# Kernel optimization log

Measured on AMD Instinct MI355X. Metric: run time of the kernel, lower is better.

## Reference

```python
import jax, jax.numpy as jnp
import numpy as np

NUM_HEADS = 8
HEAD_DIM = 16


def setup_inputs() -> dict:
    key = jax.random.key(0)
    ks = jax.random.split(key, 9)
    B, S, E, H = 2, 4096, 16, 128
    sc_in = 1.0 / np.sqrt(E)
    sc_h = 1.0 / np.sqrt(H)
    return {
        "x": jax.random.normal(ks[0], (B, S, E), dtype=jnp.float32),
        "wq": jax.random.normal(ks[1], (H, E), dtype=jnp.float32) * sc_in,
        "bq": jax.random.normal(ks[2], (H,), dtype=jnp.float32) * 0.02,
        "wk": jax.random.normal(ks[3], (H, E), dtype=jnp.float32) * sc_in,
        "bk": jax.random.normal(ks[4], (H,), dtype=jnp.float32) * 0.02,
        "wv": jax.random.normal(ks[5], (H, E), dtype=jnp.float32) * sc_in,
        "bv": jax.random.normal(ks[6], (H,), dtype=jnp.float32) * 0.02,
        "wo": jax.random.normal(ks[7], (E, H), dtype=jnp.float32) * sc_h,
        "bo": jax.random.normal(ks[8], (E,), dtype=jnp.float32) * 0.02,
    }


def reference(x, wq, bq, wk, bk, wv, bv, wo, bo):
    B, S, E = x.shape
    H = wq.shape[0]
    nh, hd = NUM_HEADS, HEAD_DIM
    # QKV projections (torch Linear: y = x @ W.T + b)
    q = x @ wq.T + bq  # [B,S,H]
    k = x @ wk.T + bk
    v = x @ wv.T + bv
    # split heads -> [B,nh,S,hd]
    q = q.reshape(B, S, nh, hd).transpose(0, 2, 1, 3)
    k = k.reshape(B, S, nh, hd).transpose(0, 2, 1, 3)
    v = v.reshape(B, S, nh, hd).transpose(0, 2, 1, 3)
    # flex_attention with block_mask=None == full SDPA, scale = 1/sqrt(head_dim)
    scale = 1.0 / np.sqrt(hd)
    scores = jnp.einsum("bhqd,bhkd->bhqk", q, k) * scale  # [B,nh,S,S]
    attn = jax.nn.softmax(scores, axis=-1)
    out = jnp.einsum("bhqk,bhkd->bhqd", attn, v)  # [B,nh,S,hd]
    out = out.transpose(0, 2, 1, 3).reshape(B, S, H)
    return out @ wo.T + bo
```

## Files before the change

kernel.cpp:

```cpp
#include <hip/hip_runtime.h>
#include <hip/hip_bf16.h>
#include <math.h>

#define NH 8
#define HD 16
#define EE 16
#define HH 128
#define NCH 4
#define QR 32

typedef __attribute__((ext_vector_type(8)))  short short8;
typedef __attribute__((ext_vector_type(16))) float f32x16;
typedef __attribute__((ext_vector_type(4)))  float f32x4;

#define EXP2F(x) __builtin_amdgcn_exp2f(x)

__global__ __launch_bounds__(256) void qkv_fused(
        const float* __restrict__ x,
        const float* __restrict__ wq, const float* __restrict__ bq,
        const float* __restrict__ wk, const float* __restrict__ bk,
        const float* __restrict__ wv, const float* __restrict__ bv,
        __hip_bfloat16* __restrict__ Qb, __hip_bfloat16* __restrict__ Kb,
        __hip_bfloat16* __restrict__ Vt, int S) {
    int row0 = blockIdx.x * QR;
    int b = row0 / S, s0 = row0 - b * S;
    int tid = threadIdx.x;

    __shared__ __align__(16) float xs[QR][EE];
    __shared__ short vsb[QR][130];

    ((float*)xs)[tid]       = x[(size_t)row0 * EE + tid];
    ((float*)xs)[tid + 256] = x[(size_t)row0 * EE + tid + 256];
    __syncthreads();

    int h = tid & 127, sub = tid >> 7;
    float wqr[16], wkr[16], wvr[16];
    const float4* wq4 = (const float4*)(wq + h * EE);
    const float4* wk4 = (const float4*)(wk + h * EE);
    const float4* wv4 = (const float4*)(wv + h * EE);
#pragma unroll
    for (int j = 0; j < 4; ++j) {
        float4 a = wq4[j]; wqr[4*j]=a.x; wqr[4*j+1]=a.y; wqr[4*j+2]=a.z; wqr[4*j+3]=a.w;
        float4 c = wk4[j]; wkr[4*j]=c.x; wkr[4*j+1]=c.y; wkr[4*j+2]=c.z; wkr[4*j+3]=c.w;
        float4 d = wv4[j]; wvr[4*j]=d.x; wvr[4*j+1]=d.y; wvr[4*j+2]=d.z; wvr[4*j+3]=d.w;
    }
    float bqv = bq[h], bkv = bk[h], bvv = bv[h];
    int head = h >> 4, dd = h & 15;
    size_t qkbase = ((size_t)(b * NH + head) * S + s0) * HD + dd;

#pragma unroll
    for (int rr = 0; rr < 16; ++rr) {
        int r = (sub << 4) + rr;
        const float4* xv = (const float4*)xs[r];
        float aq = bqv, ak = bkv, av = bvv;
#pragma unroll
        for (int j = 0; j < 4; ++j) {
            float4 xe = xv[j];
            aq += xe.x*wqr[4*j] + xe.y*wqr[4*j+1] + xe.z*wqr[4*j+2] + xe.w*wqr[4*j+3];
            ak += xe.x*wkr[4*j] + xe.y*wkr[4*j+1] + xe.z*wkr[4*j+2] + xe.w*wkr[4*j+3];
            av += xe.x*wvr[4*j] + xe.y*wvr[4*j+1] + xe.z*wvr[4*j+2] + xe.w*wvr[4*j+3];
        }
        Qb[qkbase + (size_t)r * HD] = __float2bfloat16(aq * 0.36067376022f);
        Kb[qkbase + (size_t)r * HD] = __float2bfloat16(ak);
        __hip_bfloat16 vb = __float2bfloat16(av);
        vsb[r][h] = *reinterpret_cast<short*>(&vb);
    }
    __syncthreads();

    int hd_idx = tid >> 1;
    int head2 = hd_idx >> 4, d2 = hd_idx & 15;
    int si0 = (tid & 1) * 16;
    short8 w0, w1;
#pragma unroll
    for (int j = 0; j < 8; ++j) w0[j] = vsb[si0 + j][hd_idx];
#pragma unroll
    for (int j = 0; j < 8; ++j) w1[j] = vsb[si0 + 8 + j][hd_idx];
    short* dst = (short*)Vt + ((size_t)(b * NH + head2) * HD + d2) * S + s0 + si0;
    *(short8*)dst = w0;
    *(short8*)(dst + 8) = w1;
}

__global__ __launch_bounds__(128) void attn(const __hip_bfloat16* __restrict__ Qb,
                                            const __hip_bfloat16* __restrict__ Kb,
                                            const __hip_bfloat16* __restrict__ Vtb,
                                            float* __restrict__ Opart,
                                            float* __restrict__ Lsum,
                                            int S, int BH) {
    int bh = blockIdx.y;
    int cb = blockIdx.z;
    int wid = threadIdx.x >> 6;
    int lane = threadIdx.x & 63;
    int q0 = (blockIdx.x * 2 + wid) * 32;
    int ql = lane & 31, half = lane >> 5;
    int l15 = lane & 15, l4 = lane >> 4;
    int CS = S / NCH;
    int kbeg = cb * CS;

    __shared__ __align__(16) short Pt[2][32 * 40];
    short* pt = Pt[wid];

    const short* qptr = (const short*)Qb + ((size_t)bh * S + q0) * HD;
    const short* kf_ptr = (const short*)Kb + ((size_t)bh * S + kbeg + ql) * HD + 8 * half;
    const short* vf_ptr = (const short*)Vtb + ((size_t)bh * HD + l15) * S + kbeg + 8 * l4;

    short8 qf = *(const short8*)(qptr + ql * HD + 8 * half);

    f32x16 zc;
#pragma unroll
    for (int i = 0; i < 16; ++i) zc[i] = 0.f;

    float l = 0.f;
    f32x4 o0, o1;
#pragma unroll
    for (int i = 0; i < 4; ++i) { o0[i] = 0.f; o1[i] = 0.f; }

    for (int it = 0; it < CS / 32; ++it) {
        short8 kf = *(const short8*)kf_ptr;
        kf_ptr += 32 * HD;
        f32x16 st = __builtin_amdgcn_mfma_f32_32x32x16_bf16(kf, qf, zc, 0, 0, 0);

        float pf[16];
#pragma unroll
        for (int r = 0; r < 16; ++r) pf[r] = EXP2F(st[r]);
        float rs = ((pf[0] + pf[1]) + (pf[2] + pf[3])) + ((pf[4] + pf[5]) + (pf[6] + pf[7]))
                 + ((pf[8] + pf[9]) + (pf[10] + pf[11])) + ((pf[12] + pf[13]) + (pf[14] + pf[15]));
        l += rs;

        union PU { __hip_bfloat162 b2; unsigned u; };
        unsigned pk[8];
#pragma unroll
        for (int i = 0; i < 8; ++i) {
            float2 f2; f2.x = pf[2 * i]; f2.y = pf[2 * i + 1];
            PU pu; pu.b2 = __float22bfloat162_rn(f2);
            pk[i] = pu.u;
        }
#pragma unroll
        for (int i = 0; i < 4; ++i) {
            uint2 w; w.x = pk[2 * i]; w.y = pk[2 * i + 1];
            *(uint2*)&pt[ql * 40 + 8 * i + 4 * half] = w;
        }
        short8 p0 = *(const short8*)&pt[l15 * 40 + 8 * l4];
        short8 p1 = *(const short8*)&pt[(l15 + 16) * 40 + 8 * l4];
        short8 vf = *(const short8*)vf_ptr;
        vf_ptr += 32;

        o0 = __builtin_amdgcn_mfma_f32_16x16x32_bf16(vf, p0, o0, 0, 0, 0);
        o1 = __builtin_amdgcn_mfma_f32_16x16x32_bf16(vf, p1, o1, 0, 0, 0);
    }

    l += __shfl_xor(l, 32);

    size_t base = ((size_t)(cb * BH + bh) * S);
    float* op0 = Opart + (base + q0 + l15) * HD + 4 * l4;
    float* op1 = Opart + (base + q0 + l15 + 16) * HD + 4 * l4;
    float4 r0; r0.x = o0[0]; r0.y = o0[1]; r0.z = o0[2]; r0.w = o0[3];
    float4 r1; r1.x = o1[0]; r1.y = o1[1]; r1.z = o1[2]; r1.w = o1[3];
    *(float4*)op0 = r0;
    *(float4*)op1 = r1;
    if (half == 0) Lsum[base + q0 + ql] = l;
}

__global__ __launch_bounds__(256) void combine_proj(
        const float* __restrict__ Opart, const float* __restrict__ Lsum,
        const float* __restrict__ wo, const float* __restrict__ bo,
        float* __restrict__ out, int S, int BH) {
    int r0 = blockIdx.x * 16;
    int b = r0 / S, s0 = r0 - b * S;
    int tid = threadIdx.x;
    __shared__ float As[16][HH + 1];
    __shared__ float ws[EE][HH + 1];
#pragma unroll
    for (int i = 0; i < 8; ++i) {
        int idx = tid + i * 256;
        ws[idx >> 7][idx & 127] = wo[idx];
    }
    if (tid < 128) {
        int r = tid & 15, head = tid >> 4;
        size_t BHS = (size_t)BH * S;
        size_t base = (size_t)(b * NH + head) * S + s0 + r;
        float l = 0.f;
        float acc[HD];
#pragma unroll
        for (int d = 0; d < HD; ++d) acc[d] = 0.f;
#pragma unroll
        for (int c = 0; c < NCH; ++c) {
            l += Lsum[c * BHS + base];
            const float* op = Opart + (c * BHS + base) * HD;
#pragma unroll
            for (int d = 0; d < HD; d += 4) {
                float4 v = *(const float4*)&op[d];
                acc[d] += v.x; acc[d+1] += v.y; acc[d+2] += v.z; acc[d+3] += v.w;
            }
        }
        float inv = 1.f / l;
#pragma unroll
        for (int d = 0; d < HD; ++d) As[r][head * HD + d] = acc[d] * inv;
    }
    __syncthreads();
    int r = tid >> 4, e = tid & 15;
    float acc = bo[e];
#pragma unroll
    for (int h = 0; h < HH; ++h) acc += As[r][h] * ws[e][h];
    out[(size_t)(r0 + r) * EE + e] = acc;
}

extern "C" void kernel_launch(void* const* d_in, const int* in_sizes, int n_in,
                              void* d_out, int out_size, void* d_ws, size_t ws_size,
                              hipStream_t stream) {
    const float* x  = (const float*)d_in[0];
    const float* wq = (const float*)d_in[1];
    const float* bq = (const float*)d_in[2];
    const float* wk = (const float*)d_in[3];
    const float* bk = (const float*)d_in[4];
    const float* wv = (const float*)d_in[5];
    const float* bv = (const float*)d_in[6];
    const float* wo = (const float*)d_in[7];
    const float* bo = (const float*)d_in[8];
    float* out = (float*)d_out;

    int rows = in_sizes[0] / EE;
    int S = 4096;
    int B = rows / S;
    int BH = B * NH;

    size_t n = (size_t)rows * HH;
    __hip_bfloat16* Qb = (__hip_bfloat16*)d_ws;
    __hip_bfloat16* Kb = Qb + n;
    __hip_bfloat16* Vt = Kb + n;
    float* Opart = (float*)(Vt + n);
    float* Lsum = Opart + (size_t)NCH * BH * S * HD;

    qkv_fused<<<rows / QR, 256, 0, stream>>>(x, wq, bq, wk, bk, wv, bv, Qb, Kb, Vt, S);
    dim3 g2(S / 64, BH, NCH);
    attn<<<g2, 128, 0, stream>>>(Qb, Kb, Vt, Opart, Lsum, S, BH);
    combine_proj<<<rows / 16, 256, 0, stream>>>(Opart, Lsum, wo, bo, out, S, BH);
}
```

Measured before the change: 139.1 us.

## Reduce split-K attention partials in shared memory and stage Q/K stores

The attention kernel now assigns the four key chunks to four waves of one block and combines their partial outputs and row sums in shared memory. It writes normalized attention output directly, so the Opart/Lsum round trip through global memory goes away and the combine kernel shrinks to a plain output projection. The QKV kernel also stages Q and K in shared memory so each thread writes 16-byte vectors instead of scattered 2-byte stores. The cost is more shared memory in the QKV kernel, plus an extra block-wide barrier and larger blocks in the attention kernel.

```diff
diff --git a/kernel.cpp b/kernel.cpp
--- a/kernel.cpp
+++ b/kernel.cpp
@@ -27,7 +27,9 @@
     int tid = threadIdx.x;
 
     __shared__ __align__(16) float xs[QR][EE];
-    __shared__ short vsb[QR][130];
+    __shared__ __align__(16) short qsb[QR][136];
+    __shared__ __align__(16) short ksb[QR][136];
+    __shared__ __align__(16) short vsb[QR][136];
 
     ((float*)xs)[tid]       = x[(size_t)row0 * EE + tid];
     ((float*)xs)[tid + 256] = x[(size_t)row0 * EE + tid + 256];
@@ -45,8 +47,6 @@
         float4 d = wv4[j]; wvr[4*j]=d.x; wvr[4*j+1]=d.y; wvr[4*j+2]=d.z; wvr[4*j+3]=d.w;
     }
     float bqv = bq[h], bkv = bk[h], bvv = bv[h];
-    int head = h >> 4, dd = h & 15;
-    size_t qkbase = ((size_t)(b * NH + head) * S + s0) * HD + dd;
 
 #pragma unroll
     for (int rr = 0; rr < 16; ++rr) {
@@ -60,44 +60,62 @@
             ak += xe.x*wkr[4*j] + xe.y*wkr[4*j+1] + xe.z*wkr[4*j+2] + xe.w*wkr[4*j+3];
             av += xe.x*wvr[4*j] + xe.y*wvr[4*j+1] + xe.z*wvr[4*j+2] + xe.w*wvr[4*j+3];
         }
-        Qb[qkbase + (size_t)r * HD] = __float2bfloat16(aq * 0.36067376022f);
-        Kb[qkbase + (size_t)r * HD] = __float2bfloat16(ak);
+        __hip_bfloat16 qb = __float2bfloat16(aq * 0.36067376022f);
+        __hip_bfloat16 kb = __float2bfloat16(ak);
         __hip_bfloat16 vb = __float2bfloat16(av);
+        qsb[r][h] = *reinterpret_cast<short*>(&qb);
+        ksb[r][h] = *reinterpret_cast<short*>(&kb);
         vsb[r][h] = *reinterpret_cast<short*>(&vb);
     }
     __syncthreads();
 
-    int hd_idx = tid >> 1;
-    int head2 = hd_idx >> 4, d2 = hd_idx & 15;
-    int si0 = (tid & 1) * 16;
-    short8 w0, w1;
-#pragma unroll
-    for (int j = 0; j < 8; ++j) w0[j] = vsb[si0 + j][hd_idx];
-#pragma unroll
-    for (int j = 0; j < 8; ++j) w1[j] = vsb[si0 + 8 + j][hd_idx];
-    short* dst = (short*)Vt + ((size_t)(b * NH + head2) * HD + d2) * S + s0 + si0;
-    *(short8*)dst = w0;
-    *(short8*)(dst + 8) = w1;
-}
-
-__global__ __launch_bounds__(128) void attn(const __hip_bfloat16* __restrict__ Qb,
-                                            const __hip_bfloat16* __restrict__ Kb,
-                                            const __hip_bfloat16* __restrict__ Vtb,
-                                            float* __restrict__ Opart,
-                                            float* __restrict__ Lsum,
-                                            int S, int BH) {
+    {
+        int r = tid & 31, head = tid >> 5;
+        short8 a = *(const short8*)&qsb[r][head * 16];
+        short8 c = *(const short8*)&qsb[r][head * 16 + 8];
+        short* dst = (short*)Qb + ((size_t)(b * NH + head) * S + s0 + r) * HD;
+        *(short8*)dst = a;
+        *(short8*)(dst + 8) = c;
+        a = *(const short8*)&ksb[r][head * 16];
+        c = *(const short8*)&ksb[r][head * 16 + 8];
+        dst = (short*)Kb + ((size_t)(b * NH + head) * S + s0 + r) * HD;
+        *(short8*)dst = a;
+        *(short8*)(dst + 8) = c;
+    }
+    {
+        int hd_idx = tid >> 1;
+        int head2 = hd_idx >> 4, d2 = hd_idx & 15;
+        int si0 = (tid & 1) * 16;
+        short8 w0, w1;
+#pragma unroll
+        for (int j = 0; j < 8; ++j) w0[j] = vsb[si0 + j][hd_idx];
+#pragma unroll
+        for (int j = 0; j < 8; ++j) w1[j] = vsb[si0 + 8 + j][hd_idx];
+        short* dst = (short*)Vt + ((size_t)(b * NH + head2) * HD + d2) * S + s0 + si0;
+        *(short8*)dst = w0;
+        *(short8*)(dst + 8) = w1;
+    }
+}
+
+__global__ __launch_bounds__(256, 8) void attn(const __hip_bfloat16* __restrict__ Qb,
+                                               const __hip_bfloat16* __restrict__ Kb,
+                                               const __hip_bfloat16* __restrict__ Vtb,
+                                               float* __restrict__ A,
+                                               int S, int BH) {
     int bh = blockIdx.y;
-    int cb = blockIdx.z;
-    int wid = threadIdx.x >> 6;
+    int q0 = blockIdx.x * 32;
+    int cb = threadIdx.x >> 6;
     int lane = threadIdx.x & 63;
-    int q0 = (blockIdx.x * 2 + wid) * 32;
     int ql = lane & 31, half = lane >> 5;
     int l15 = lane & 15, l4 = lane >> 4;
     int CS = S / NCH;
     int kbeg = cb * CS;
 
-    __shared__ __align__(16) short Pt[2][32 * 40];
-    short* pt = Pt[wid];
+    __shared__ __align__(16) union {
+        short pt[NCH][32 * 40];
+        struct { float o[NCH][32][16]; float l[NCH][32]; } red;
+    } sm;
+    short* pt = sm.pt[cb];
 
     const short* qptr = (const short*)Qb + ((size_t)bh * S + q0) * HD;
     const short* kf_ptr = (const short*)Kb + ((size_t)bh * S + kbeg + ql) * HD + 8 * half;
@@ -150,51 +168,45 @@
 
     l += __shfl_xor(l, 32);
 
-    size_t base = ((size_t)(cb * BH + bh) * S);
-    float* op0 = Opart + (base + q0 + l15) * HD + 4 * l4;
-    float* op1 = Opart + (base + q0 + l15 + 16) * HD + 4 * l4;
-    float4 r0; r0.x = o0[0]; r0.y = o0[1]; r0.z = o0[2]; r0.w = o0[3];
-    float4 r1; r1.x = o1[0]; r1.y = o1[1]; r1.z = o1[2]; r1.w = o1[3];
-    *(float4*)op0 = r0;
-    *(float4*)op1 = r1;
-    if (half == 0) Lsum[base + q0 + ql] = l;
-}
-
-__global__ __launch_bounds__(256) void combine_proj(
-        const float* __restrict__ Opart, const float* __restrict__ Lsum,
-        const float* __restrict__ wo, const float* __restrict__ bo,
-        float* __restrict__ out, int S, int BH) {
-    int r0 = blockIdx.x * 16;
-    int b = r0 / S, s0 = r0 - b * S;
-    int tid = threadIdx.x;
+    __syncthreads();
+    {
+        float4 r0; r0.x = o0[0]; r0.y = o0[1]; r0.z = o0[2]; r0.w = o0[3];
+        float4 r1; r1.x = o1[0]; r1.y = o1[1]; r1.z = o1[2]; r1.w = o1[3];
+        *(float4*)&sm.red.o[cb][l15][4 * l4]      = r0;
+        *(float4*)&sm.red.o[cb][l15 + 16][4 * l4] = r1;
+        if (half == 0) sm.red.l[cb][ql] = l;
+    }
+    __syncthreads();
+
+    if (threadIdx.x < 128) {
+        int q = threadIdx.x >> 2, quad = threadIdx.x & 3;
+        float4 acc; acc.x = 0.f; acc.y = 0.f; acc.z = 0.f; acc.w = 0.f;
+        float ls = 0.f;
+#pragma unroll
+        for (int c = 0; c < NCH; ++c) {
+            float4 v = *(const float4*)&sm.red.o[c][q][4 * quad];
+            acc.x += v.x; acc.y += v.y; acc.z += v.z; acc.w += v.w;
+            ls += sm.red.l[c][q];
+        }
+        float inv = 1.f / ls;
+        acc.x *= inv; acc.y *= inv; acc.z *= inv; acc.w *= inv;
+        int b = bh >> 3, head = bh & 7;
+        *(float4*)&A[((size_t)(b * S + q0 + q)) * HH + head * HD + 4 * quad] = acc;
+    }
+}
+
+__global__ __launch_bounds__(256) void out_proj(
+        const float* __restrict__ A, const float* __restrict__ wo,
+        const float* __restrict__ bo, float* __restrict__ out, int rows) {
     __shared__ float As[16][HH + 1];
     __shared__ float ws[EE][HH + 1];
+    int r0 = blockIdx.x * 16;
+    int tid = threadIdx.x;
 #pragma unroll
     for (int i = 0; i < 8; ++i) {
         int idx = tid + i * 256;
         ws[idx >> 7][idx & 127] = wo[idx];
-    }
-    if (tid < 128) {
-        int r = tid & 15, head = tid >> 4;
-        size_t BHS = (size_t)BH * S;
-        size_t base = (size_t)(b * NH + head) * S + s0 + r;
-        float l = 0.f;
-        float acc[HD];
-#pragma unroll
-        for (int d = 0; d < HD; ++d) acc[d] = 0.f;
-#pragma unroll
-        for (int c = 0; c < NCH; ++c) {
-            l += Lsum[c * BHS + base];
-            const float* op = Opart + (c * BHS + base) * HD;
-#pragma unroll
-            for (int d = 0; d < HD; d += 4) {
-                float4 v = *(const float4*)&op[d];
-                acc[d] += v.x; acc[d+1] += v.y; acc[d+2] += v.z; acc[d+3] += v.w;
-            }
-        }
-        float inv = 1.f / l;
-#pragma unroll
-        for (int d = 0; d < HD; ++d) As[r][head * HD + d] = acc[d] * inv;
+        As[idx >> 7][idx & 127] = A[(size_t)r0 * HH + idx];
     }
     __syncthreads();
     int r = tid >> 4, e = tid & 15;
@@ -227,11 +239,10 @@
     __hip_bfloat16* Qb = (__hip_bfloat16*)d_ws;
     __hip_bfloat16* Kb = Qb + n;
     __hip_bfloat16* Vt = Kb + n;
-    float* Opart = (float*)(Vt + n);
-    float* Lsum = Opart + (size_t)NCH * BH * S * HD;
+    float* A = (float*)(Vt + n);
 
     qkv_fused<<<rows / QR, 256, 0, stream>>>(x, wq, bq, wk, bk, wv, bv, Qb, Kb, Vt, S);
-    dim3 g2(S / 64, BH, NCH);
-    attn<<<g2, 128, 0, stream>>>(Qb, Kb, Vt, Opart, Lsum, S, BH);
-    combine_proj<<<rows / 16, 256, 0, stream>>>(Opart, Lsum, wo, bo, out, S, BH);
-}
+    dim3 g2(S / 32, BH);
+    attn<<<g2, 256, 0, stream>>>(Qb, Kb, Vt, A, S, BH);
+    out_proj<<<rows / 16, 256, 0, stream>>>(A, wo, bo, out, rows);
+}
```

After: 129.0 us. 7.3% less time.
